# Performance work log

Hardware: AMD Instinct MI355X
Metric: run time of the kernel (lower is better)

Reference implementation:

```python
import jax, jax.numpy as jnp
import numpy as np


def setup_inputs() -> dict:
    key = jax.random.key(0)
    k1, k2, k3 = jax.random.split(key, 3)
    B, H, S, D = 2, 8, 4096, 64
    queries = jax.random.normal(k1, (B, H, S, D), dtype=jnp.float32)
    keys = jax.random.normal(k2, (B, H, S, D), dtype=jnp.float32)
    values = jax.random.normal(k3, (B, H, S, D), dtype=jnp.float32)
    mask = jnp.zeros((1, 1, S, S), dtype=jnp.float32)
    return {"queries": queries, "keys": keys, "values": values, "d_k": D, "mask": mask}


def reference(queries, keys, values, d_k, mask):
    # scores: [B, H, Sq, Sk]
    scale = 1.0 / jnp.sqrt(jnp.asarray(d_k, dtype=queries.dtype))
    scores = jnp.einsum("bhqd,bhkd->bhqk", queries, keys) * scale
    scores = scores + (-1e9) * mask  # additive mask, broadcasts over B, H
    weights = jax.nn.softmax(scores, axis=-1)
    return jnp.einsum("bhqk,bhkd->bhqd", weights, values)
```

## Files before the change

kernel.cpp:

```cpp
#include <hip/hip_runtime.h>

#define S_LEN 4096
#define DHEAD 64
#define BQ    64
#define BK    64
#define KPAD  72

typedef __fp16   pk16x2 __attribute__((ext_vector_type(2)));
typedef _Float16 half4v __attribute__((ext_vector_type(4)));
typedef _Float16 half8  __attribute__((ext_vector_type(8)));
typedef float    f32x4  __attribute__((ext_vector_type(4)));

__global__ void mask_flag_kernel(const float4* __restrict__ mask, int* __restrict__ flag) {
    const long stride = 2048L * 256;
    long i = (long)blockIdx.x * 256 + threadIdx.x;
    int nz = 0;
    #pragma unroll
    for (int it = 0; it < 8; ++it) {
        float4 a = mask[i + it * stride];
        nz |= (a.x != 0.f) | (a.y != 0.f) | (a.z != 0.f) | (a.w != 0.f);
    }
    if (__any(nz)) {
        if ((threadIdx.x & 63) == 0) atomicOr(flag, 1);
    }
}

__global__ __launch_bounds__(256, 4) void attn_kernel(
    const float* __restrict__ Q, const float* __restrict__ K,
    const float* __restrict__ V, const int* __restrict__ dk,
    const float* __restrict__ mask, const int* __restrict__ maskflag,
    float* __restrict__ O)
{
    const int qt   = blockIdx.x;
    const int bh   = blockIdx.y;
    const int tid  = threadIdx.x;
    const int wave = tid >> 6;
    const int lane = tid & 63;
    const int l15  = lane & 15;
    const int quad = lane >> 4;

    const long base = (long)bh * S_LEN * DHEAD;
    const float* Qh = Q + base;
    const float* Kh = K + base;
    const float* Vh = V + base;
    float*       Oh = O + base;

    const int q0 = qt * BQ + wave * 16;
    const float csq  = rsqrtf((float)dk[0]) * 1.44269504088896f;
    const float mfac = -1e9f * 1.44269504088896f;
    const bool use_mask = (maskflag[0] != 0);

    __shared__ __align__(16) _Float16 Kt[BK][KPAD];
    __shared__ __align__(16) _Float16 Vt[DHEAD * KPAD];
    __shared__ __align__(16) _Float16 Pw[4][16][KPAD];

    half8 qf[2];
    #pragma unroll
    for (int kc = 0; kc < 2; ++kc) {
        const float4* src = (const float4*)(Qh + (long)(q0 + l15) * DHEAD + kc*32 + quad*8);
        float4 a = src[0], b = src[1];
        union { pk16x2 p[4]; half8 h; } u;
        u.p[0] = __builtin_amdgcn_cvt_pkrtz(a.x*csq, a.y*csq);
        u.p[1] = __builtin_amdgcn_cvt_pkrtz(a.z*csq, a.w*csq);
        u.p[2] = __builtin_amdgcn_cvt_pkrtz(b.x*csq, b.y*csq);
        u.p[3] = __builtin_amdgcn_cvt_pkrtz(b.z*csq, b.w*csq);
        qf[kc] = u.h;
    }

    const int kr  = tid >> 2;
    const int ks  = tid & 3;
    const int vrp = tid >> 3;
    const int vdq = tid & 7;
    const float* Kb = Kh + (long)kr * DHEAD + ks * 16;
    const float* Vb = Vh + (long)(2 * vrp) * DHEAD + vdq * 8;
    const int vcol = (((vrp >> 2) ^ vdq) << 3) + ((2 * vrp) & 7);
    const int vd0  = vdq * 8;

    float4 kf[4], vf[4];
    auto load_tile = [&](int kt) {
        const float4* kp  = (const float4*)(Kb + (long)kt * BK * DHEAD);
        kf[0] = kp[0]; kf[1] = kp[1]; kf[2] = kp[2]; kf[3] = kp[3];
        const float4* vp0 = (const float4*)(Vb + (long)kt * BK * DHEAD);
        const float4* vp1 = (const float4*)(Vb + (long)kt * BK * DHEAD + DHEAD);
        vf[0] = vp0[0]; vf[1] = vp0[1]; vf[2] = vp1[0]; vf[3] = vp1[1];
    };
    auto store_tile = [&]() {
        union { pk16x2 p[4]; half8 h; } u0, u1;
        u0.p[0] = __builtin_amdgcn_cvt_pkrtz(kf[0].x, kf[0].y);
        u0.p[1] = __builtin_amdgcn_cvt_pkrtz(kf[0].z, kf[0].w);
        u0.p[2] = __builtin_amdgcn_cvt_pkrtz(kf[1].x, kf[1].y);
        u0.p[3] = __builtin_amdgcn_cvt_pkrtz(kf[1].z, kf[1].w);
        u1.p[0] = __builtin_amdgcn_cvt_pkrtz(kf[2].x, kf[2].y);
        u1.p[1] = __builtin_amdgcn_cvt_pkrtz(kf[2].z, kf[2].w);
        u1.p[2] = __builtin_amdgcn_cvt_pkrtz(kf[3].x, kf[3].y);
        u1.p[3] = __builtin_amdgcn_cvt_pkrtz(kf[3].z, kf[3].w);
        *(half8*)&Kt[kr][ks*16]     = u0.h;
        *(half8*)&Kt[kr][ks*16 + 8] = u1.h;
        *(pk16x2*)&Vt[(vd0+0)*KPAD + vcol] = __builtin_amdgcn_cvt_pkrtz(vf[0].x, vf[2].x);
        *(pk16x2*)&Vt[(vd0+1)*KPAD + vcol] = __builtin_amdgcn_cvt_pkrtz(vf[0].y, vf[2].y);
        *(pk16x2*)&Vt[(vd0+2)*KPAD + vcol] = __builtin_amdgcn_cvt_pkrtz(vf[0].z, vf[2].z);
        *(pk16x2*)&Vt[(vd0+3)*KPAD + vcol] = __builtin_amdgcn_cvt_pkrtz(vf[0].w, vf[2].w);
        *(pk16x2*)&Vt[(vd0+4)*KPAD + vcol] = __builtin_amdgcn_cvt_pkrtz(vf[1].x, vf[3].x);
        *(pk16x2*)&Vt[(vd0+5)*KPAD + vcol] = __builtin_amdgcn_cvt_pkrtz(vf[1].y, vf[3].y);
        *(pk16x2*)&Vt[(vd0+6)*KPAD + vcol] = __builtin_amdgcn_cvt_pkrtz(vf[1].z, vf[3].z);
        *(pk16x2*)&Vt[(vd0+7)*KPAD + vcol] = __builtin_amdgcn_cvt_pkrtz(vf[1].w, vf[3].w);
    };

    f32x4 o[4];
    #pragma unroll
    for (int dt = 0; dt < 4; ++dt) o[dt] = (f32x4){0.f, 0.f, 0.f, 0.f};
    float m_i = -INFINITY;
    float l_i = 0.0f;

    load_tile(0);
    for (int kt = 0; kt < S_LEN / BK; ++kt) {
        store_tile();
        __syncthreads();
        if (kt + 1 < S_LEN / BK) load_tile(kt + 1);

        f32x4 st[4];
        #pragma unroll
        for (int nt = 0; nt < 4; ++nt) st[nt] = (f32x4){0.f,0.f,0.f,0.f};
        #pragma unroll
        for (int nt = 0; nt < 4; ++nt) {
            #pragma unroll
            for (int kc = 0; kc < 2; ++kc) {
                half8 af = *(const half8*)&Kt[nt*16 + l15][kc*32 + quad*8];
                st[nt] = __builtin_amdgcn_mfma_f32_16x16x32_f16(af, qf[kc], st[nt], 0, 0, 0);
            }
        }

        if (use_mask) {
            const long mrow = (long)(q0 + l15) * S_LEN + kt*BK;
            #pragma unroll
            for (int nt = 0; nt < 4; ++nt)
                #pragma unroll
                for (int r = 0; r < 4; ++r)
                    st[nt][r] += mfac * mask[mrow + nt*16 + quad*4 + r];
        }

        float mx = fmaxf(fmaxf(fmaxf(st[0][0], st[0][1]), fmaxf(st[0][2], st[0][3])),
                         fmaxf(fmaxf(st[1][0], st[1][1]), fmaxf(st[1][2], st[1][3])));
        float mx2 = fmaxf(fmaxf(fmaxf(st[2][0], st[2][1]), fmaxf(st[2][2], st[2][3])),
                          fmaxf(fmaxf(st[3][0], st[3][1]), fmaxf(st[3][2], st[3][3])));
        mx = fmaxf(mx, mx2);
        mx = fmaxf(mx, __shfl_xor(mx, 16, 64));
        mx = fmaxf(mx, __shfl_xor(mx, 32, 64));
        float mnew = fmaxf(m_i, mx);
        float rsum = 0.0f;
        #pragma unroll
        for (int nt = 0; nt < 4; ++nt) {
            #pragma unroll
            for (int r = 0; r < 4; ++r) {
                float p = __builtin_amdgcn_exp2f(st[nt][r] - mnew);
                st[nt][r] = p;
                rsum += p;
            }
        }
        rsum += __shfl_xor(rsum, 16, 64);
        rsum += __shfl_xor(rsum, 32, 64);
        float alpha = __builtin_amdgcn_exp2f(m_i - mnew);
        l_i = alpha * l_i + rsum;
        m_i = mnew;

        #pragma unroll
        for (int r = 0; r < 4; ++r) {
            float a_r = __shfl(alpha, quad*4 + r, 64);
            #pragma unroll
            for (int dt = 0; dt < 4; ++dt) o[dt][r] *= a_r;
        }

        #pragma unroll
        for (int nt = 0; nt < 4; ++nt) {
            union { pk16x2 p[2]; half4v h; } up;
            up.p[0] = __builtin_amdgcn_cvt_pkrtz(st[nt][0], st[nt][1]);
            up.p[1] = __builtin_amdgcn_cvt_pkrtz(st[nt][2], st[nt][3]);
            *(half4v*)&Pw[wave][l15][nt*16 + quad*4] = up.h;
        }
        #pragma unroll
        for (int kc2 = 0; kc2 < 2; ++kc2) {
            half8 pa = *(const half8*)&Pw[wave][l15][kc2*32 + quad*8];
            #pragma unroll
            for (int dt = 0; dt < 4; ++dt) {
                const int row = dt*16 + l15;
                const int pb  = (4*kc2 + quad) ^ (row >> 3);
                half8 vb = *(const half8*)&Vt[row*KPAD + pb*8];
                o[dt] = __builtin_amdgcn_mfma_f32_16x16x32_f16(pa, vb, o[dt], 0, 0, 0);
            }
        }
        __syncthreads();
    }

    float linv[4];
    #pragma unroll
    for (int r = 0; r < 4; ++r) {
        float lq = __shfl(l_i, quad*4 + r, 64);
        linv[r] = __builtin_amdgcn_rcpf(lq);
    }
    #pragma unroll
    for (int r = 0; r < 4; ++r) {
        const long row = (long)(q0 + quad*4 + r) * DHEAD;
        #pragma unroll
        for (int dt = 0; dt < 4; ++dt)
            Oh[row + dt*16 + l15] = o[dt][r] * linv[r];
    }
}

extern "C" void kernel_launch(void* const* d_in, const int* in_sizes, int n_in,
                              void* d_out, int out_size, void* d_ws, size_t ws_size,
                              hipStream_t stream) {
    const float* Q    = (const float*)d_in[0];
    const float* K    = (const float*)d_in[1];
    const float* V    = (const float*)d_in[2];
    const int*   dk   = (const int*)d_in[3];
    const float* mask = (const float*)d_in[4];
    float* out = (float*)d_out;
    int* flag = (int*)d_ws;

    (void)hipMemsetAsync(flag, 0, sizeof(int), stream);
    mask_flag_kernel<<<2048, 256, 0, stream>>>((const float4*)mask, flag);

    dim3 grid(S_LEN / BQ, 16);
    attn_kernel<<<grid, 256, 0, stream>>>(Q, K, V, dk, mask, flag, out);
}
```

Measured before the change: 283.8 us.

## Double query rows per wave and double-buffer K/V tiles in LDS

Each wave now handles two 16-row query fragments (BQ 128), so every K/V fragment read from LDS feeds two MFMAs, halving K/V global and LDS traffic per query. K/V shared tiles are double-buffered, which removes one of the two barriers per iteration and lets the next tile's store overlap with compute. The cost is more registers (launch bounds lowered to 2 blocks/CU), more LDS, and half as many blocks (512 blocks on 256 CUs), which may hurt occupancy and latency hiding.

```diff
diff --git a/kernel.cpp b/kernel.cpp
--- a/kernel.cpp
+++ b/kernel.cpp
@@ -2,8 +2,9 @@
 
 #define S_LEN 4096
 #define DHEAD 64
-#define BQ    64
+#define BQ    128
 #define BK    64
+#define NT    (S_LEN / BK)
 #define KPAD  72
 
 typedef __fp16   pk16x2 __attribute__((ext_vector_type(2)));
@@ -25,7 +26,7 @@
     }
 }
 
-__global__ __launch_bounds__(256, 4) void attn_kernel(
+__global__ __launch_bounds__(256, 2) void attn_kernel(
     const float* __restrict__ Q, const float* __restrict__ K,
     const float* __restrict__ V, const int* __restrict__ dk,
     const float* __restrict__ mask, const int* __restrict__ maskflag,
@@ -45,26 +46,29 @@
     const float* Vh = V + base;
     float*       Oh = O + base;
 
-    const int q0 = qt * BQ + wave * 16;
+    const int q0 = qt * BQ + wave * 32;
     const float csq  = rsqrtf((float)dk[0]) * 1.44269504088896f;
     const float mfac = -1e9f * 1.44269504088896f;
     const bool use_mask = (maskflag[0] != 0);
 
-    __shared__ __align__(16) _Float16 Kt[BK][KPAD];
-    __shared__ __align__(16) _Float16 Vt[DHEAD * KPAD];
-    __shared__ __align__(16) _Float16 Pw[4][16][KPAD];
-
-    half8 qf[2];
-    #pragma unroll
-    for (int kc = 0; kc < 2; ++kc) {
-        const float4* src = (const float4*)(Qh + (long)(q0 + l15) * DHEAD + kc*32 + quad*8);
-        float4 a = src[0], b = src[1];
-        union { pk16x2 p[4]; half8 h; } u;
-        u.p[0] = __builtin_amdgcn_cvt_pkrtz(a.x*csq, a.y*csq);
-        u.p[1] = __builtin_amdgcn_cvt_pkrtz(a.z*csq, a.w*csq);
-        u.p[2] = __builtin_amdgcn_cvt_pkrtz(b.x*csq, b.y*csq);
-        u.p[3] = __builtin_amdgcn_cvt_pkrtz(b.z*csq, b.w*csq);
-        qf[kc] = u.h;
+    __shared__ __align__(16) _Float16 Kt[2][BK][KPAD];
+    __shared__ __align__(16) _Float16 Vt[2][DHEAD * KPAD];
+    __shared__ __align__(16) _Float16 Pw[4][32][KPAD];
+
+    half8 qf[2][2];
+    #pragma unroll
+    for (int f = 0; f < 2; ++f) {
+        #pragma unroll
+        for (int kc = 0; kc < 2; ++kc) {
+            const float4* src = (const float4*)(Qh + (long)(q0 + f*16 + l15) * DHEAD + kc*32 + quad*8);
+            float4 a = src[0], b = src[1];
+            union { pk16x2 p[4]; half8 h; } u;
+            u.p[0] = __builtin_amdgcn_cvt_pkrtz(a.x*csq, a.y*csq);
+            u.p[1] = __builtin_amdgcn_cvt_pkrtz(a.z*csq, a.w*csq);
+            u.p[2] = __builtin_amdgcn_cvt_pkrtz(b.x*csq, b.y*csq);
+            u.p[3] = __builtin_amdgcn_cvt_pkrtz(b.z*csq, b.w*csq);
+            qf[f][kc] = u.h;
+        }
     }
 
     const int kr  = tid >> 2;
@@ -84,7 +88,7 @@
         const float4* vp1 = (const float4*)(Vb + (long)kt * BK * DHEAD + DHEAD);
         vf[0] = vp0[0]; vf[1] = vp0[1]; vf[2] = vp1[0]; vf[3] = vp1[1];
     };
-    auto store_tile = [&]() {
+    auto store_tile = [&](int b) {
         union { pk16x2 p[4]; half8 h; } u0, u1;
         u0.p[0] = __builtin_amdgcn_cvt_pkrtz(kf[0].x, kf[0].y);
         u0.p[1] = __builtin_amdgcn_cvt_pkrtz(kf[0].z, kf[0].w);
@@ -94,115 +98,140 @@
         u1.p[1] = __builtin_amdgcn_cvt_pkrtz(kf[2].z, kf[2].w);
         u1.p[2] = __builtin_amdgcn_cvt_pkrtz(kf[3].x, kf[3].y);
         u1.p[3] = __builtin_amdgcn_cvt_pkrtz(kf[3].z, kf[3].w);
-        *(half8*)&Kt[kr][ks*16]     = u0.h;
-        *(half8*)&Kt[kr][ks*16 + 8] = u1.h;
-        *(pk16x2*)&Vt[(vd0+0)*KPAD + vcol] = __builtin_amdgcn_cvt_pkrtz(vf[0].x, vf[2].x);
-        *(pk16x2*)&Vt[(vd0+1)*KPAD + vcol] = __builtin_amdgcn_cvt_pkrtz(vf[0].y, vf[2].y);
-        *(pk16x2*)&Vt[(vd0+2)*KPAD + vcol] = __builtin_amdgcn_cvt_pkrtz(vf[0].z, vf[2].z);
-        *(pk16x2*)&Vt[(vd0+3)*KPAD + vcol] = __builtin_amdgcn_cvt_pkrtz(vf[0].w, vf[2].w);
-        *(pk16x2*)&Vt[(vd0+4)*KPAD + vcol] = __builtin_amdgcn_cvt_pkrtz(vf[1].x, vf[3].x);
-        *(pk16x2*)&Vt[(vd0+5)*KPAD + vcol] = __builtin_amdgcn_cvt_pkrtz(vf[1].y, vf[3].y);
-        *(pk16x2*)&Vt[(vd0+6)*KPAD + vcol] = __builtin_amdgcn_cvt_pkrtz(vf[1].z, vf[3].z);
-        *(pk16x2*)&Vt[(vd0+7)*KPAD + vcol] = __builtin_amdgcn_cvt_pkrtz(vf[1].w, vf[3].w);
+        *(half8*)&Kt[b][kr][ks*16]     = u0.h;
+        *(half8*)&Kt[b][kr][ks*16 + 8] = u1.h;
+        _Float16* vt = &Vt[b][0];
+        *(pk16x2*)&vt[(vd0+0)*KPAD + vcol] = __builtin_amdgcn_cvt_pkrtz(vf[0].x, vf[2].x);
+        *(pk16x2*)&vt[(vd0+1)*KPAD + vcol] = __builtin_amdgcn_cvt_pkrtz(vf[0].y, vf[2].y);
+        *(pk16x2*)&vt[(vd0+2)*KPAD + vcol] = __builtin_amdgcn_cvt_pkrtz(vf[0].z, vf[2].z);
+        *(pk16x2*)&vt[(vd0+3)*KPAD + vcol] = __builtin_amdgcn_cvt_pkrtz(vf[0].w, vf[2].w);
+        *(pk16x2*)&vt[(vd0+4)*KPAD + vcol] = __builtin_amdgcn_cvt_pkrtz(vf[1].x, vf[3].x);
+        *(pk16x2*)&vt[(vd0+5)*KPAD + vcol] = __builtin_amdgcn_cvt_pkrtz(vf[1].y, vf[3].y);
+        *(pk16x2*)&vt[(vd0+6)*KPAD + vcol] = __builtin_amdgcn_cvt_pkrtz(vf[1].z, vf[3].z);
+        *(pk16x2*)&vt[(vd0+7)*KPAD + vcol] = __builtin_amdgcn_cvt_pkrtz(vf[1].w, vf[3].w);
     };
 
-    f32x4 o[4];
-    #pragma unroll
-    for (int dt = 0; dt < 4; ++dt) o[dt] = (f32x4){0.f, 0.f, 0.f, 0.f};
-    float m_i = -INFINITY;
-    float l_i = 0.0f;
+    f32x4 o[2][4];
+    #pragma unroll
+    for (int f = 0; f < 2; ++f)
+        #pragma unroll
+        for (int dt = 0; dt < 4; ++dt) o[f][dt] = (f32x4){0.f, 0.f, 0.f, 0.f};
+    float m_i[2] = {-INFINITY, -INFINITY};
+    float l_i[2] = {0.0f, 0.0f};
 
     load_tile(0);
-    for (int kt = 0; kt < S_LEN / BK; ++kt) {
-        store_tile();
-        __syncthreads();
-        if (kt + 1 < S_LEN / BK) load_tile(kt + 1);
-
-        f32x4 st[4];
-        #pragma unroll
-        for (int nt = 0; nt < 4; ++nt) st[nt] = (f32x4){0.f,0.f,0.f,0.f};
+    store_tile(0);
+    __syncthreads();
+
+    for (int kt = 0; kt < NT; ++kt) {
+        const int b = kt & 1;
+        if (kt + 1 < NT) load_tile(kt + 1);
+
+        f32x4 st[2][4];
+        #pragma unroll
+        for (int f = 0; f < 2; ++f)
+            #pragma unroll
+            for (int nt = 0; nt < 4; ++nt) st[f][nt] = (f32x4){0.f,0.f,0.f,0.f};
         #pragma unroll
         for (int nt = 0; nt < 4; ++nt) {
             #pragma unroll
             for (int kc = 0; kc < 2; ++kc) {
-                half8 af = *(const half8*)&Kt[nt*16 + l15][kc*32 + quad*8];
-                st[nt] = __builtin_amdgcn_mfma_f32_16x16x32_f16(af, qf[kc], st[nt], 0, 0, 0);
+                half8 af = *(const half8*)&Kt[b][nt*16 + l15][kc*32 + quad*8];
+                st[0][nt] = __builtin_amdgcn_mfma_f32_16x16x32_f16(af, qf[0][kc], st[0][nt], 0, 0, 0);
+                st[1][nt] = __builtin_amdgcn_mfma_f32_16x16x32_f16(af, qf[1][kc], st[1][nt], 0, 0, 0);
             }
         }
 
         if (use_mask) {
-            const long mrow = (long)(q0 + l15) * S_LEN + kt*BK;
-            #pragma unroll
-            for (int nt = 0; nt < 4; ++nt)
+            #pragma unroll
+            for (int f = 0; f < 2; ++f) {
+                const long mrow = (long)(q0 + f*16 + l15) * S_LEN + kt*BK;
                 #pragma unroll
-                for (int r = 0; r < 4; ++r)
-                    st[nt][r] += mfac * mask[mrow + nt*16 + quad*4 + r];
-        }
-
-        float mx = fmaxf(fmaxf(fmaxf(st[0][0], st[0][1]), fmaxf(st[0][2], st[0][3])),
-                         fmaxf(fmaxf(st[1][0], st[1][1]), fmaxf(st[1][2], st[1][3])));
-        float mx2 = fmaxf(fmaxf(fmaxf(st[2][0], st[2][1]), fmaxf(st[2][2], st[2][3])),
-                          fmaxf(fmaxf(st[3][0], st[3][1]), fmaxf(st[3][2], st[3][3])));
-        mx = fmaxf(mx, mx2);
-        mx = fmaxf(mx, __shfl_xor(mx, 16, 64));
-        mx = fmaxf(mx, __shfl_xor(mx, 32, 64));
-        float mnew = fmaxf(m_i, mx);
-        float rsum = 0.0f;
-        #pragma unroll
-        for (int nt = 0; nt < 4; ++nt) {
+                for (int nt = 0; nt < 4; ++nt)
+                    #pragma unroll
+                    for (int r = 0; r < 4; ++r)
+                        st[f][nt][r] += mfac * mask[mrow + nt*16 + quad*4 + r];
+            }
+        }
+
+        float alpha[2];
+        #pragma unroll
+        for (int f = 0; f < 2; ++f) {
+            float mx = fmaxf(fmaxf(fmaxf(st[f][0][0], st[f][0][1]), fmaxf(st[f][0][2], st[f][0][3])),
+                             fmaxf(fmaxf(st[f][1][0], st[f][1][1]), fmaxf(st[f][1][2], st[f][1][3])));
+            float mx2 = fmaxf(fmaxf(fmaxf(st[f][2][0], st[f][2][1]), fmaxf(st[f][2][2], st[f][2][3])),
+                              fmaxf(fmaxf(st[f][3][0], st[f][3][1]), fmaxf(st[f][3][2], st[f][3][3])));
+            mx = fmaxf(mx, mx2);
+            mx = fmaxf(mx, __shfl_xor(mx, 16, 64));
+            mx = fmaxf(mx, __shfl_xor(mx, 32, 64));
+            float mnew = fmaxf(m_i[f], mx);
+            float rsum = 0.0f;
+            #pragma unroll
+            for (int nt = 0; nt < 4; ++nt) {
+                #pragma unroll
+                for (int r = 0; r < 4; ++r) {
+                    float p = __builtin_amdgcn_exp2f(st[f][nt][r] - mnew);
+                    st[f][nt][r] = p;
+                    rsum += p;
+                }
+            }
+            rsum += __shfl_xor(rsum, 16, 64);
+            rsum += __shfl_xor(rsum, 32, 64);
+            alpha[f] = __builtin_amdgcn_exp2f(m_i[f] - mnew);
+            l_i[f] = alpha[f] * l_i[f] + rsum;
+            m_i[f] = mnew;
+        }
+
+        #pragma unroll
+        for (int f = 0; f < 2; ++f)
             #pragma unroll
             for (int r = 0; r < 4; ++r) {
-                float p = __builtin_amdgcn_exp2f(st[nt][r] - mnew);
-                st[nt][r] = p;
-                rsum += p;
-            }
-        }
-        rsum += __shfl_xor(rsum, 16, 64);
-        rsum += __shfl_xor(rsum, 32, 64);
-        float alpha = __builtin_amdgcn_exp2f(m_i - mnew);
-        l_i = alpha * l_i + rsum;
-        m_i = mnew;
-
-        #pragma unroll
-        for (int r = 0; r < 4; ++r) {
-            float a_r = __shfl(alpha, quad*4 + r, 64);
-            #pragma unroll
-            for (int dt = 0; dt < 4; ++dt) o[dt][r] *= a_r;
-        }
-
-        #pragma unroll
-        for (int nt = 0; nt < 4; ++nt) {
-            union { pk16x2 p[2]; half4v h; } up;
-            up.p[0] = __builtin_amdgcn_cvt_pkrtz(st[nt][0], st[nt][1]);
-            up.p[1] = __builtin_amdgcn_cvt_pkrtz(st[nt][2], st[nt][3]);
-            *(half4v*)&Pw[wave][l15][nt*16 + quad*4] = up.h;
-        }
+                float a_r = __shfl(alpha[f], quad*4 + r, 64);
+                #pragma unroll
+                for (int dt = 0; dt < 4; ++dt) o[f][dt][r] *= a_r;
+            }
+
+        #pragma unroll
+        for (int f = 0; f < 2; ++f)
+            #pragma unroll
+            for (int nt = 0; nt < 4; ++nt) {
+                union { pk16x2 p[2]; half4v h; } up;
+                up.p[0] = __builtin_amdgcn_cvt_pkrtz(st[f][nt][0], st[f][nt][1]);
+                up.p[1] = __builtin_amdgcn_cvt_pkrtz(st[f][nt][2], st[f][nt][3]);
+                *(half4v*)&Pw[wave][f*16 + l15][nt*16 + quad*4] = up.h;
+            }
+
         #pragma unroll
         for (int kc2 = 0; kc2 < 2; ++kc2) {
-            half8 pa = *(const half8*)&Pw[wave][l15][kc2*32 + quad*8];
+            half8 pa0 = *(const half8*)&Pw[wave][l15][kc2*32 + quad*8];
+            half8 pa1 = *(const half8*)&Pw[wave][16 + l15][kc2*32 + quad*8];
             #pragma unroll
             for (int dt = 0; dt < 4; ++dt) {
                 const int row = dt*16 + l15;
                 const int pb  = (4*kc2 + quad) ^ (row >> 3);
-                half8 vb = *(const half8*)&Vt[row*KPAD + pb*8];
-                o[dt] = __builtin_amdgcn_mfma_f32_16x16x32_f16(pa, vb, o[dt], 0, 0, 0);
-            }
-        }
-        __syncthreads();
-    }
-
-    float linv[4];
-    #pragma unroll
-    for (int r = 0; r < 4; ++r) {
-        float lq = __shfl(l_i, quad*4 + r, 64);
-        linv[r] = __builtin_amdgcn_rcpf(lq);
-    }
-    #pragma unroll
-    for (int r = 0; r < 4; ++r) {
-        const long row = (long)(q0 + quad*4 + r) * DHEAD;
-        #pragma unroll
-        for (int dt = 0; dt < 4; ++dt)
-            Oh[row + dt*16 + l15] = o[dt][r] * linv[r];
+                half8 vb = *(const half8*)&Vt[b][row*KPAD + pb*8];
+                o[0][dt] = __builtin_amdgcn_mfma_f32_16x16x32_f16(pa0, vb, o[0][dt], 0, 0, 0);
+                o[1][dt] = __builtin_amdgcn_mfma_f32_16x16x32_f16(pa1, vb, o[1][dt], 0, 0, 0);
+            }
+        }
+
+        if (kt + 1 < NT) {
+            store_tile((kt + 1) & 1);
+            __syncthreads();
+        }
+    }
+
+    #pragma unroll
+    for (int f = 0; f < 2; ++f) {
+        #pragma unroll
+        for (int r = 0; r < 4; ++r) {
+            float lq = __shfl(l_i[f], quad*4 + r, 64);
+            float linv = __builtin_amdgcn_rcpf(lq);
+            const long row = (long)(q0 + f*16 + quad*4 + r) * DHEAD;
+            #pragma unroll
+            for (int dt = 0; dt < 4; ++dt)
+                Oh[row + dt*16 + l15] = o[f][dt][r] * linv;
+        }
     }
 }
 
```

New measurement: 258.1 us. 1.1x faster.
